# Kernel tuning notes

Hardware: AMD Instinct MI355X
Metric: run time of the kernel (lower is better)

The kernel has to match this reference:

```python
import jax, jax.numpy as jnp
import numpy as np

N = 8192        # num neurons
D = 512         # neuron_state_size
NEG = -1e30     # finite mask value (avoids inf-inf NaNs, matches empty-predecessor -> zero output)


def setup_inputs() -> dict:
    key = jax.random.key(0)
    ks = jax.random.split(key, 5)
    neuron_states = jax.random.normal(ks[0], (N, D), dtype=jnp.float32)
    # sparse-ish directed adjacency; adjacency[i, j] True => i is a predecessor of j
    adjacency = jax.random.bernoulli(ks[1], 0.05, (N, N))
    Wq = jax.random.normal(ks[2], (D, D), dtype=jnp.float32) / np.sqrt(D)
    Wk = jax.random.normal(ks[3], (D, D), dtype=jnp.float32) / np.sqrt(D)
    Wv = jax.random.normal(ks[4], (D, D), dtype=jnp.float32) / np.sqrt(D)
    return {"neuron_states": neuron_states, "adjacency": adjacency, "Wq": Wq, "Wk": Wk, "Wv": Wv}


def reference(neuron_states, adjacency, Wq, Wk, Wv):
    # nn.Linear(bias=False): y = x @ W.T
    q = neuron_states @ Wq.T          # [N, D]
    k = neuron_states @ Wk.T          # [N, D]
    v = neuron_states @ Wv.T          # [N, D]
    # score[j, i] = q_j . k_i, valid iff adjacency[i, j] (i is predecessor of j)
    mask = adjacency.T                # [N_dst, N_src]
    scores = jnp.where(mask, q @ k.T, NEG)
    attn = jax.nn.softmax(scores, axis=1)
    attn = jnp.where(mask, attn, 0.0)  # neurons with no predecessors -> zero output (matches torch empty matmul)
    return attn @ v                   # [N, D]
```

## Files before the change

### kernel.cpp

```cpp
#include <hip/hip_runtime.h>
#include <stdint.h>

#define N 8192
#define D 512
#define NEG -1e30f

typedef _Float16 f16;
typedef f16 f16x4 __attribute__((ext_vector_type(4)));
typedef f16 f16x8 __attribute__((ext_vector_type(8)));
typedef float f32x4v __attribute__((ext_vector_type(4)));
typedef float f32x16 __attribute__((ext_vector_type(16)));

#define XH_OFF   0ull
#define WQH_OFF  (XH_OFF + 8192ull * 512 * 2)
#define WKH_OFF  (WQH_OFF + 512ull * 512 * 2)
#define WVH_OFF  (WKH_OFF + 512ull * 512 * 2)
#define QH_OFF   (WVH_OFF + 512ull * 512 * 2)
#define KH_OFF   (QH_OFF + 8192ull * 512 * 2)
#define VT_OFF   (KH_OFF + 8192ull * 512 * 2)
#define PART_SZ  (8192ull * 512 * 2)
#define P123_OFF (VT_OFF + 8192ull * 512 * 2)

#define QROW     1040
#define QS_OFF   0
#define PROW     144
#define PSB_OFF  66560
#define MLXM_OFF (PSB_OFF + 64 * PROW)
#define MLXL_OFF (MLXM_OFF + 1024)
#define MROW_OFF (MLXL_OFF + 1024)
#define LROW_OFF (MROW_OFF + 256)
#define SCL_OFF  (LROW_OFF + 256)
#define LDSB_V4  (SCL_OFF + 256)

__global__ __launch_bounds__(256) void cvt_fp16(
    const float* __restrict__ X,
    const float* __restrict__ Wq, const float* __restrict__ Wk, const float* __restrict__ Wv,
    f16* __restrict__ Xh,
    f16* __restrict__ Wqh, f16* __restrict__ Wkh, f16* __restrict__ Wvh)
{
    const int idx = blockIdx.x * 256 + threadIdx.x;
    const float* src; f16* dst; int off;
    if (idx < 1048576)      { src = X;  dst = Xh;  off = idx; }
    else if (idx < 1114112) { src = Wq; dst = Wqh; off = idx - 1048576; }
    else if (idx < 1179648) { src = Wk; dst = Wkh; off = idx - 1114112; }
    else                    { src = Wv; dst = Wvh; off = idx - 1179648; }
    const float4 v = ((const float4*)src)[off];
    f16x4 h; h.x = (f16)v.x; h.y = (f16)v.y; h.z = (f16)v.z; h.w = (f16)v.w;
    *(f16x4*)(dst + (size_t)off * 4) = h;
}

__global__ __launch_bounds__(256) void qkv_mfma(
    const f16* __restrict__ Xh,
    const f16* __restrict__ Wqh, const f16* __restrict__ Wkh, const f16* __restrict__ Wvh,
    f16* __restrict__ qh, f16* __restrict__ kh, f16* __restrict__ vt)
{
    const int t    = threadIdx.x;
    const int w    = t >> 6;
    const int lane = t & 63;
    const int lo   = lane & 31;
    const int hi   = lane >> 5;
    const int z    = blockIdx.z;

    int m0, c0; const f16 *Ap, *Bp; f16* Yp; size_t ldy;
    if (z == 2) {
        m0 = blockIdx.x * 128 + w * 32; c0 = blockIdx.y * 128;
        Ap = Wvh; Bp = Xh; Yp = vt; ldy = N;
    } else {
        m0 = blockIdx.y * 128 + w * 32; c0 = blockIdx.x * 128;
        Ap = Xh; Bp = z ? Wkh : Wqh; Yp = z ? kh : qh; ldy = D;
    }

    const f16* arow = Ap + (size_t)(m0 + lo) * D + hi * 8;
    const f16* brow[4];
#pragma unroll
    for (int nn = 0; nn < 4; ++nn)
        brow[nn] = Bp + (size_t)(c0 + nn * 32 + lo) * D + hi * 8;

    f32x16 acc[4];
#pragma unroll
    for (int nn = 0; nn < 4; ++nn)
#pragma unroll
        for (int e = 0; e < 16; ++e) acc[nn][e] = 0.f;

#pragma unroll 4
    for (int ks = 0; ks < 32; ++ks) {
        const f16x8 a = *(const f16x8*)(arow + ks * 16);
#pragma unroll
        for (int nn = 0; nn < 4; ++nn) {
            const f16x8 b = *(const f16x8*)(brow[nn] + ks * 16);
            acc[nn] = __builtin_amdgcn_mfma_f32_32x32x16_f16(a, b, acc[nn], 0, 0, 0);
        }
    }

#pragma unroll
    for (int nn = 0; nn < 4; ++nn)
#pragma unroll
        for (int r = 0; r < 16; ++r) {
            const int row = m0 + (r & 3) + 8 * (r >> 2) + 4 * hi;
            Yp[(size_t)row * ldy + c0 + nn * 32 + lo] = (f16)acc[nn][r];
        }
}

__global__ __launch_bounds__(256, 2) void attn_v4(
    const f16* __restrict__ qh, const f16* __restrict__ kh,
    const f16* __restrict__ vt, const int* __restrict__ adj,
    f16* __restrict__ part0, f16* __restrict__ part123, float2* __restrict__ ml)
{
    extern __shared__ char smem[];
    char*  Qs   = smem + QS_OFF;
    char*  Psb  = smem + PSB_OFF;
    float* mlxm = (float*)(smem + MLXM_OFF);
    float* mlxl = (float*)(smem + MLXL_OFF);
    float* mrow = (float*)(smem + MROW_OFF);
    float* lrow = (float*)(smem + LROW_OFF);
    float* scl  = (float*)(smem + SCL_OFF);

    const int t  = threadIdx.x;
    const int w  = t >> 6;
    const int l  = t & 63;
    const int cl = l & 15;
    const int hq = l >> 4;

    const int nib = gridDim.x >> 7;
    const int b   = blockIdx.x;
    const int xcd = b & 7;
    int ib, jt_;
    if (nib == 4) { ib = xcd >> 1; jt_ = (xcd & 1) * 64 + (b >> 3); }
    else          { ib = xcd >> 2; jt_ = (xcd & 3) * 32 + (b >> 3); }
    const int j0    = jt_ * 64;
    const int ibase = ib * (N / nib);
    const int iters = (N / nib) >> 6;

    f16* pb = (ib == 0) ? part0 : part123 + (size_t)(ib - 1) * ((size_t)N * D);

    for (int c = t; c < 64 * 64; c += 256) {
        const int row = c >> 6, off = c & 63;
        f16x8 v = *(const f16x8*)(qh + (size_t)(j0 + row) * D + off * 8);
        *(f16x8*)(Qs + row * QROW + off * 16) = v;
    }
    if (t < 64) { mrow[t] = NEG; lrow[t] = 0.f; }
    __syncthreads();

    f32x4v oacc[4][8];
#pragma unroll
    for (int jt = 0; jt < 4; ++jt)
#pragma unroll
        for (int dt = 0; dt < 8; ++dt) {
            oacc[jt][dt][0] = 0.f; oacc[jt][dt][1] = 0.f;
            oacc[jt][dt][2] = 0.f; oacc[jt][dt][3] = 0.f;
        }

    const char* qbase[4];
#pragma unroll
    for (int jt = 0; jt < 4; ++jt) qbase[jt] = Qs + (jt * 16 + cl) * QROW;
    const int qoff = hq * 16;

    for (int it = 0; it < iters; ++it) {
        const int i0t = ibase + it * 64;

        f32x4v sacc[4];
#pragma unroll
        for (int jt = 0; jt < 4; ++jt) {
            sacc[jt][0] = 0.f; sacc[jt][1] = 0.f; sacc[jt][2] = 0.f; sacc[jt][3] = 0.f;
        }
        const f16* kp = kh + (size_t)(i0t + w * 16 + cl) * D + hq * 8;
#pragma unroll 4
        for (int ks = 0; ks < 16; ++ks) {
            const f16x8 kf = *(const f16x8*)(kp + ks * 32);
#pragma unroll
            for (int jt = 0; jt < 4; ++jt) {
                const f16x8 qf = *(const f16x8*)(qbase[jt] + ks * 64 + qoff);
                sacc[jt] = __builtin_amdgcn_mfma_f32_16x16x32_f16(kf, qf, sacc[jt], 0, 0, 0);
            }
        }

        const int* ap = adj + (size_t)(i0t + w * 16 + hq * 4) * N + j0 + cl;
        float pe[4][4], mb[4];
#pragma unroll
        for (int jt = 0; jt < 4; ++jt) {
            int mk[4];
#pragma unroll
            for (int r = 0; r < 4; ++r) mk[r] = ap[(size_t)r * N + jt * 16];
            float s[4];
#pragma unroll
            for (int r = 0; r < 4; ++r) s[r] = mk[r] ? sacc[jt][r] : NEG;
            float m4 = fmaxf(fmaxf(s[0], s[1]), fmaxf(s[2], s[3]));
            m4 = fmaxf(m4, __shfl_xor(m4, 16, 64));
            m4 = fmaxf(m4, __shfl_xor(m4, 32, 64));
            mb[jt] = m4;
            float pl = 0.f;
#pragma unroll
            for (int r = 0; r < 4; ++r) {
                const float p = mk[r] ? __expf(s[r] - m4) : 0.f;
                pe[jt][r] = p;
                pl += p;
            }
            pl += __shfl_xor(pl, 16, 64);
            pl += __shfl_xor(pl, 32, 64);
            if (l < 16) {
                mlxm[w * 64 + jt * 16 + l] = m4;
                mlxl[w * 64 + jt * 16 + l] = pl;
            }
        }
        __syncthreads();

        if (t < 64) {
            const float mo = mrow[t];
            const float m0b = mlxm[t],       l0b = mlxl[t];
            const float m1b = mlxm[64 + t],  l1b = mlxl[64 + t];
            const float m2b = mlxm[128 + t], l2b = mlxl[128 + t];
            const float m3b = mlxm[192 + t], l3b = mlxl[192 + t];
            const float mn = fmaxf(mo, fmaxf(fmaxf(m0b, m1b), fmaxf(m2b, m3b)));
            const float ln = lrow[t] * __expf(mo - mn)
                           + l0b * __expf(m0b - mn) + l1b * __expf(m1b - mn)
                           + l2b * __expf(m2b - mn) + l3b * __expf(m3b - mn);
            mrow[t] = mn; lrow[t] = ln; scl[t] = __expf(mo - mn);
        }
        __syncthreads();

#pragma unroll
        for (int jt = 0; jt < 4; ++jt) {
            const f32x4v sc4 = *(const f32x4v*)(scl + jt * 16 + hq * 4);
#pragma unroll
            for (int dt = 0; dt < 8; ++dt) {
                oacc[jt][dt][0] *= sc4[0]; oacc[jt][dt][1] *= sc4[1];
                oacc[jt][dt][2] *= sc4[2]; oacc[jt][dt][3] *= sc4[3];
            }
            const float mn = mrow[jt * 16 + cl];
            const float f  = __expf(mb[jt] - mn);
            union { f16 h[4]; uint2 u; } pc;
#pragma unroll
            for (int r = 0; r < 4; ++r) pc.h[r] = (f16)(pe[jt][r] * f);
            *(uint2*)(Psb + (jt * 16 + cl) * PROW + (w * 16 + hq * 4) * 2) = pc.u;
        }
        __syncthreads();

        f16x8 pa[4][2];
#pragma unroll
        for (int jt = 0; jt < 4; ++jt)
#pragma unroll
            for (int k2 = 0; k2 < 2; ++k2)
                pa[jt][k2] = *(const f16x8*)(Psb + (jt * 16 + cl) * PROW + k2 * 64 + hq * 16);

#pragma unroll
        for (int dt = 0; dt < 8; ++dt) {
            const f16* vp = vt + (size_t)(w * 128 + dt * 16 + cl) * N + i0t + hq * 8;
#pragma unroll
            for (int k2 = 0; k2 < 2; ++k2) {
                const f16x8 vf = *(const f16x8*)(vp + k2 * 32);
#pragma unroll
                for (int jt = 0; jt < 4; ++jt)
                    oacc[jt][dt] = __builtin_amdgcn_mfma_f32_16x16x32_f16(pa[jt][k2], vf, oacc[jt][dt], 0, 0, 0);
            }
        }
        __syncthreads();
    }

#pragma unroll
    for (int jt = 0; jt < 4; ++jt)
#pragma unroll
        for (int dt = 0; dt < 8; ++dt)
#pragma unroll
            for (int r = 0; r < 4; ++r)
                pb[(size_t)(j0 + jt * 16 + hq * 4 + r) * D + w * 128 + dt * 16 + cl] =
                    (f16)oacc[jt][dt][r];
    if (t < 64) {
        float2 v; v.x = mrow[t]; v.y = lrow[t];
        ml[(size_t)ib * N + j0 + t] = v;
    }
}

__global__ __launch_bounds__(256) void merge_p(
    float* __restrict__ out, const f16* __restrict__ p0,
    const f16* __restrict__ p123, const float2* __restrict__ ml, int nib)
{
    const int idx = blockIdx.x * 256 + threadIdx.x;
    const int j = idx >> 7;
    const int col = (idx & 127) * 4;

    float m_g = NEG;
    for (int ib = 0; ib < nib; ++ib) m_g = fmaxf(m_g, ml[(size_t)ib * N + j].x);
    float L = 0.f;
    float4 acc; acc.x = 0.f; acc.y = 0.f; acc.z = 0.f; acc.w = 0.f;
    for (int ib = 0; ib < nib; ++ib) {
        const float2 a = ml[(size_t)ib * N + j];
        const float e = __expf(a.x - m_g);
        L += e * a.y;
        const f16* pp = (ib == 0) ? p0 : p123 + (size_t)(ib - 1) * ((size_t)N * D);
        const f16x4 h = *(const f16x4*)(pp + (size_t)j * D + col);
        acc.x += e * (float)h.x; acc.y += e * (float)h.y;
        acc.z += e * (float)h.z; acc.w += e * (float)h.w;
    }
    const float inv = (L > 0.f) ? 1.f / L : 0.f;
    float4 r; r.x = acc.x * inv; r.y = acc.y * inv; r.z = acc.z * inv; r.w = acc.w * inv;
    ((float4*)out)[idx] = r;
}

extern "C" void kernel_launch(void* const* d_in, const int* in_sizes, int n_in,
                              void* d_out, int out_size, void* d_ws, size_t ws_size,
                              hipStream_t stream) {
    const float* ns  = (const float*)d_in[0];
    const int*   adj = (const int*)d_in[1];
    const float* Wq  = (const float*)d_in[2];
    const float* Wk  = (const float*)d_in[3];
    const float* Wv  = (const float*)d_in[4];

    char* ws = (char*)d_ws;
    f16*   Xh   = (f16*)(ws + XH_OFF);
    f16*   Wqh  = (f16*)(ws + WQH_OFF);
    f16*   Wkh  = (f16*)(ws + WKH_OFF);
    f16*   Wvh  = (f16*)(ws + WVH_OFF);
    f16*   qh   = (f16*)(ws + QH_OFF);
    f16*   kh   = (f16*)(ws + KH_OFF);
    f16*   vt   = (f16*)(ws + VT_OFF);
    f16*   p0   = (f16*)(ws + XH_OFF);
    f16*   p123 = (f16*)(ws + P123_OFF);
    float* out  = (float*)d_out;

    const size_t need4 = P123_OFF + 3 * PART_SZ + 4ull * N * sizeof(float2);
    int nib; size_t ml_off;
    if (ws_size >= need4) { nib = 4; ml_off = P123_OFF + 3 * PART_SZ; }
    else                  { nib = 2; ml_off = P123_OFF + 1 * PART_SZ; }
    float2* mlb = (float2*)(ws + ml_off);

    (void)hipFuncSetAttribute((const void*)attn_v4,
                              hipFuncAttributeMaxDynamicSharedMemorySize, LDSB_V4);

    cvt_fp16<<<4864, 256, 0, stream>>>(ns, Wq, Wk, Wv, Xh, Wqh, Wkh, Wvh);
    qkv_mfma<<<dim3(4, 64, 3), 256, 0, stream>>>(Xh, Wqh, Wkh, Wvh, qh, kh, vt);
    attn_v4<<<128 * nib, 256, LDSB_V4, stream>>>(qh, kh, vt, adj, p0, p123, mlb);
    merge_p<<<4096, 256, 0, stream>>>(out, p0, p123, mlb, nib);
}
```

Before: 443.7 us.

## Pack adjacency mask into 64-bit bitmasks before attention kernel

Adds a pack_adj pre-pass that turns the int32 adjacency matrix into one 64-bit word per (64-source block, destination), stored in workspace. The attention kernel then reads one u64 per column tile instead of four int loads per tile row, which cuts mask traffic in the inner loop, and the exp guard now tests the masked score rather than the mask. The cost is an extra kernel that still reads the full 256MB int matrix once, with poorly coalesced column-strided reads, plus a larger workspace requirement that may force the nib=2 fallback.

```diff
diff --git a/kernel.cpp b/kernel.cpp
--- a/kernel.cpp
+++ b/kernel.cpp
@@ -10,6 +10,7 @@
 typedef f16 f16x8 __attribute__((ext_vector_type(8)));
 typedef float f32x4v __attribute__((ext_vector_type(4)));
 typedef float f32x16 __attribute__((ext_vector_type(16)));
+typedef unsigned long long u64;
 
 #define XH_OFF   0ull
 #define WQH_OFF  (XH_OFF + 8192ull * 512 * 2)
@@ -20,6 +21,8 @@
 #define VT_OFF   (KH_OFF + 8192ull * 512 * 2)
 #define PART_SZ  (8192ull * 512 * 2)
 #define P123_OFF (VT_OFF + 8192ull * 512 * 2)
+#define ML_SZ    (4ull * N * 8)
+#define ADJ_SZ   (128ull * N * 8)
 
 #define QROW     1040
 #define QS_OFF   0
@@ -101,9 +104,23 @@
         }
 }
 
+__global__ __launch_bounds__(256) void pack_adj(
+    const int* __restrict__ adj, u64* __restrict__ adjb)
+{
+    const int idx = blockIdx.x * 256 + threadIdx.x;
+    const int j   = idx & (N - 1);
+    const int iw  = idx >> 13;
+    const int* src = adj + (size_t)iw * 64 * N + j;
+    u64 bits = 0;
+#pragma unroll 8
+    for (int i2 = 0; i2 < 64; ++i2)
+        bits |= (u64)(src[(size_t)i2 * N] != 0) << i2;
+    adjb[(size_t)iw * N + j] = bits;
+}
+
 __global__ __launch_bounds__(256, 2) void attn_v4(
     const f16* __restrict__ qh, const f16* __restrict__ kh,
-    const f16* __restrict__ vt, const int* __restrict__ adj,
+    const f16* __restrict__ vt, const u64* __restrict__ adjb,
     f16* __restrict__ part0, f16* __restrict__ part123, float2* __restrict__ ml)
 {
     extern __shared__ char smem[];
@@ -158,6 +175,13 @@
     for (int it = 0; it < iters; ++it) {
         const int i0t = ibase + it * 64;
 
+        u64 wd[4];
+        {
+            const u64* ab = adjb + ((size_t)(i0t >> 6)) * N + j0 + cl;
+#pragma unroll
+            for (int jt = 0; jt < 4; ++jt) wd[jt] = ab[jt * 16];
+        }
+
         f32x4v sacc[4];
 #pragma unroll
         for (int jt = 0; jt < 4; ++jt) {
@@ -174,16 +198,13 @@
             }
         }
 
-        const int* ap = adj + (size_t)(i0t + w * 16 + hq * 4) * N + j0 + cl;
         float pe[4][4], mb[4];
 #pragma unroll
         for (int jt = 0; jt < 4; ++jt) {
-            int mk[4];
-#pragma unroll
-            for (int r = 0; r < 4; ++r) mk[r] = ap[(size_t)r * N + jt * 16];
+            const uint32_t sub = (uint32_t)(wd[jt] >> (w * 16 + hq * 4)) & 0xFu;
             float s[4];
 #pragma unroll
-            for (int r = 0; r < 4; ++r) s[r] = mk[r] ? sacc[jt][r] : NEG;
+            for (int r = 0; r < 4; ++r) s[r] = ((sub >> r) & 1) ? sacc[jt][r] : NEG;
             float m4 = fmaxf(fmaxf(s[0], s[1]), fmaxf(s[2], s[3]));
             m4 = fmaxf(m4, __shfl_xor(m4, 16, 64));
             m4 = fmaxf(m4, __shfl_xor(m4, 32, 64));
@@ -191,7 +212,7 @@
             float pl = 0.f;
 #pragma unroll
             for (int r = 0; r < 4; ++r) {
-                const float p = mk[r] ? __expf(s[r] - m4) : 0.f;
+                const float p = (s[r] > -1e29f) ? __expf(s[r] - m4) : 0.f;
                 pe[jt][r] = p;
                 pl += p;
             }
@@ -317,17 +338,19 @@
     f16*   p123 = (f16*)(ws + P123_OFF);
     float* out  = (float*)d_out;
 
-    const size_t need4 = P123_OFF + 3 * PART_SZ + 4ull * N * sizeof(float2);
+    const size_t need4 = P123_OFF + 3 * PART_SZ + ML_SZ + ADJ_SZ;
     int nib; size_t ml_off;
     if (ws_size >= need4) { nib = 4; ml_off = P123_OFF + 3 * PART_SZ; }
     else                  { nib = 2; ml_off = P123_OFF + 1 * PART_SZ; }
-    float2* mlb = (float2*)(ws + ml_off);
+    float2* mlb  = (float2*)(ws + ml_off);
+    u64*    adjb = (u64*)(ws + ml_off + ML_SZ);
 
     (void)hipFuncSetAttribute((const void*)attn_v4,
                               hipFuncAttributeMaxDynamicSharedMemorySize, LDSB_V4);
 
     cvt_fp16<<<4864, 256, 0, stream>>>(ns, Wq, Wk, Wv, Xh, Wqh, Wkh, Wvh);
     qkv_mfma<<<dim3(4, 64, 3), 256, 0, stream>>>(Xh, Wqh, Wkh, Wvh, qh, kh, vt);
-    attn_v4<<<128 * nib, 256, LDSB_V4, stream>>>(qh, kh, vt, adj, p0, p123, mlb);
+    pack_adj<<<4096, 256, 0, stream>>>(adj, adjb);
+    attn_v4<<<128 * nib, 256, LDSB_V4, stream>>>(qh, kh, vt, adjb, p0, p123, mlb);
     merge_p<<<4096, 256, 0, stream>>>(out, p0, p123, mlb, nib);
 }
```

After: 432.2 us. -2.6%, faster.
